# Optimization experiments

Measured on AMD Instinct MI355X. Metric: run time of the kernel, lower is better.

## Reference

```python
import jax, jax.numpy as jnp
import numpy as np

B, N, C, H = 2, 2048, 1024, 16
D = C // H  # head_dim = 64


def setup_inputs() -> dict:
    key = jax.random.key(0)
    ks = jax.random.split(key, 5)
    s = 0.02
    return {
        "x": jax.random.normal(ks[0], (B, N, C), dtype=jnp.float32),
        "w_qkv": jax.random.normal(ks[1], (3 * C, C), dtype=jnp.float32) * s,
        "b_qkv": jnp.zeros((3 * C,), dtype=jnp.float32),
        "w_proj": jax.random.normal(ks[2], (C, C), dtype=jnp.float32) * s,
        "b_proj": jnp.zeros((C,), dtype=jnp.float32),
    }


def reference(x, w_qkv, b_qkv, w_proj, b_proj):
    scale = D ** -0.5
    # QKV projection: [B,N,3C]
    qkv = jnp.einsum('bnc,oc->bno', x, w_qkv) + b_qkv
    qkv = qkv.reshape(B, N, 3, H, D).transpose(2, 0, 3, 1, 4)  # [3,B,H,N,D]
    q, k, v = qkv[0], qkv[1], qkv[2]
    attn = jnp.einsum('bhnd,bhmd->bhnm', q, k) * scale  # [B,H,N,N]
    attn = jax.nn.softmax(attn, axis=-1)
    out = jnp.einsum('bhnm,bhmd->bhnd', attn, v)  # [B,H,N,D]
    out = out.transpose(0, 2, 1, 3).reshape(B, N, C)
    return jnp.einsum('bnc,oc->bno', out, w_proj) + b_proj
```

## Files before the change

### kernel.cpp

```cpp
#include <hip/hip_runtime.h>
#include <hip/hip_bf16.h>

typedef __attribute__((ext_vector_type(4))) float f32x4;
typedef __attribute__((ext_vector_type(16))) float f32x16;
typedef __attribute__((ext_vector_type(8))) short short8;
typedef __attribute__((ext_vector_type(4))) unsigned int u32x4;
typedef __attribute__((ext_vector_type(2))) unsigned int u32x2;
typedef unsigned short u16;

__device__ __forceinline__ u16 f2bf(float x) {
  unsigned u = __float_as_uint(x);
  u += 0x7fffu + ((u >> 16) & 1u);
  return (u16)(u >> 16);
}

__device__ __forceinline__ void gload_lds16(const void* g, void* l) {
  __builtin_amdgcn_global_load_lds(
      (__attribute__((address_space(1))) void*)g,
      (__attribute__((address_space(3))) void*)l, 16, 0, 0);
}

__global__ void cvt_all(const float* __restrict__ x, const float* __restrict__ wq,
                        const float* __restrict__ wp, ushort4* __restrict__ dst) {
  const int N1 = 1048576, N2 = 786432, NT = 2097152;
  for (int i = blockIdx.x * 256 + threadIdx.x; i < NT; i += 524288) {
    float4 v;
    if (i < N1)            v = ((const float4*)x)[i];
    else if (i < N1 + N2)  v = ((const float4*)wq)[i - N1];
    else                   v = ((const float4*)wp)[i - N1 - N2];
    ushort4 o;
    o.x = f2bf(v.x); o.y = f2bf(v.y); o.z = f2bf(v.z); o.w = f2bf(v.w);
    dst[i] = o;
  }
}

__global__ __launch_bounds__(512, 2) void gemm256_bt(
    const u16* __restrict__ A, const u16* __restrict__ B,
    const float* __restrict__ bias, u16* __restrict__ Cout,
    int M, int N, int K)
{
  __shared__ u16 LA[2][2][8192];
  __shared__ u16 LB[2][12288];

  const int tid  = threadIdx.x;
  const int w    = tid >> 6;
  const int lane = tid & 63;
  const int wm   = w >> 2;
  const int wn   = w & 3;
  const int hi   = lane >> 4;
  const int lo   = lane & 15;

  const int L  = (int)(blockIdx.x & 7) * 32 + (int)(blockIdx.x >> 3);
  const int bx = L >> 4, by = L & 15;
  const long brow = (long)by * 256;
  const long bcol = (long)bx * 192;

  f32x4 acc[8][3];
#pragma unroll
  for (int m = 0; m < 8; ++m)
#pragma unroll
    for (int n = 0; n < 3; ++n)
#pragma unroll
      for (int r = 0; r < 4; ++r) acc[m][n][r] = 0.0f;

  const int srow = lane >> 3;
  const int sg   = (lane & 7) ^ srow;
  const int l7   = lo & 7;

  auto stA = [&](int kt, int bi, int i) {
    const long k0 = (long)kt * 64;
#pragma unroll
    for (int mh = 0; mh < 2; ++mh) {
      const long r = brow + mh * 128 + i * 64 + w * 8 + srow;
      gload_lds16(A + r * K + k0 + sg * 8, &LA[bi][mh][i * 4096 + w * 512]);
    }
  };
  auto stB = [&](int kt, int bi, int u) {
    const long k0 = (long)kt * 64;
    const long r = bcol + u * 64 + w * 8 + srow;
    gload_lds16(B + r * K + k0 + sg * 8, &LB[bi][u * 4096 + w * 512]);
  };

  short8 a[4][2], b[3][2];
  auto rdA = [&](int bi, int mq) {
#pragma unroll
    for (int f = 0; f < 4; ++f) {
      const int rl = mq * 64 + f * 16 + lo;
#pragma unroll
      for (int ks = 0; ks < 2; ++ks)
        a[f][ks] = *(const short8*)(&LA[bi][wm][rl * 64 + ((ks * 4 + hi) ^ l7) * 8]);
    }
  };
  auto rdB = [&](int bi) {
#pragma unroll
    for (int f = 0; f < 3; ++f) {
      const int rl = wn * 48 + f * 16 + lo;
#pragma unroll
      for (int ks = 0; ks < 2; ++ks)
        b[f][ks] = *(const short8*)(&LB[bi][rl * 64 + ((ks * 4 + hi) ^ l7) * 8]);
    }
  };

#define MFMA24(mq)                                                                  \
  __builtin_amdgcn_s_setprio(1);                                                    \
  _Pragma("unroll")                                                                 \
  for (int f = 0; f < 4; ++f)                                                       \
    _Pragma("unroll")                                                               \
    for (int n = 0; n < 3; ++n)                                                     \
      _Pragma("unroll")                                                             \
      for (int ks = 0; ks < 2; ++ks)                                                \
        acc[(mq)*4 + f][n] = __builtin_amdgcn_mfma_f32_16x16x32_bf16(               \
            a[f][ks], b[n][ks], acc[(mq)*4 + f][n], 0, 0, 0);                       \
  __builtin_amdgcn_s_setprio(0);

#define PHASE_WAIT()                                      \
  __builtin_amdgcn_s_barrier();                           \
  asm volatile("s_waitcnt lgkmcnt(0)" ::: "memory");      \
  __builtin_amdgcn_sched_barrier(0);

  const int nkt = K >> 6;
  stA(0, 0, 0); stA(0, 0, 1); stB(0, 0, 0); stB(0, 0, 1); stB(0, 0, 2);
  stA(1, 1, 0); stA(1, 1, 1); stB(1, 1, 0); stB(1, 1, 1); stB(1, 1, 2);
  asm volatile("s_waitcnt vmcnt(7)" ::: "memory");
  __builtin_amdgcn_s_barrier();

  for (int it = 0; it < (nkt >> 1); ++it) {
    const int t2 = 2 * it + 2, t3 = 2 * it + 3;
    rdA(0, 0); rdB(0);
    if (it > 0) stA(2 * it + 1, 1, 1);
    PHASE_WAIT(); MFMA24(0); __builtin_amdgcn_s_barrier();
    rdA(0, 1);
    if (t2 < nkt) { stB(t2, 0, 0); stB(t2, 0, 1); stB(t2, 0, 2); stA(t2, 0, 0); }
    PHASE_WAIT(); MFMA24(1);
    if (t2 < nkt) { asm volatile("s_waitcnt vmcnt(5)" ::: "memory"); }
    else          { asm volatile("s_waitcnt vmcnt(0)" ::: "memory"); }
    __builtin_amdgcn_sched_barrier(0);
    __builtin_amdgcn_s_barrier();
    rdA(1, 0); rdB(1);
    if (t2 < nkt) stA(t2, 0, 1);
    PHASE_WAIT(); MFMA24(0); __builtin_amdgcn_s_barrier();
    rdA(1, 1);
    if (t3 < nkt) { stB(t3, 1, 0); stB(t3, 1, 1); stB(t3, 1, 2); stA(t3, 1, 0); }
    PHASE_WAIT(); MFMA24(1);
    if (t3 < nkt) { asm volatile("s_waitcnt vmcnt(5)" ::: "memory"); }
    __builtin_amdgcn_sched_barrier(0);
    __builtin_amdgcn_s_barrier();
  }
#undef MFMA24
#undef PHASE_WAIT

  const float SCC = 0.18033688011112042f;
  float bv[3];
#pragma unroll
  for (int n = 0; n < 3; ++n) bv[n] = bias[bcol + wn * 48 + n * 16 + lo];
#pragma unroll
  for (int m = 0; m < 8; ++m)
#pragma unroll
    for (int n = 0; n < 3; ++n) {
      const long colf = bcol + wn * 48 + n * 16;
      const float qsc = (colf < 1024) ? SCC : 1.0f;
#pragma unroll
      for (int r = 0; r < 4; ++r) {
        const long row = brow + wm * 128 + m * 16 + hi * 4 + r;
        Cout[row * (long)N + colf + lo] = f2bf((acc[m][n][r] + bv[n]) * qsc);
      }
    }
}

template<int OUT_BF16>
__global__ __launch_bounds__(256) void gemm_bt(
    const u16* __restrict__ A, const u16* __restrict__ B,
    const float* __restrict__ bias, void* __restrict__ Cout,
    int M, int N, int K)
{
  __shared__ u16 As[2][128 * 64];
  __shared__ u16 Bs[2][128 * 64];
  const int tid  = threadIdx.x;
  const int lane = tid & 63;
  const int w    = tid >> 6;
  const int wm   = w >> 1, wn = w & 1;
  const int hi   = lane >> 4;
  const int lo   = lane & 15;
  const int l7   = lo & 7;
  const long brow = (long)blockIdx.y * 128;
  const long bcol = (long)blockIdx.x * 128;

  f32x4 acc[4][4];
#pragma unroll
  for (int i = 0; i < 4; i++)
#pragma unroll
    for (int j = 0; j < 4; j++)
#pragma unroll
      for (int r = 0; r < 4; r++) acc[i][j][r] = 0.0f;

  const int srow = lane >> 3;
  const int sg   = (lane & 7) ^ srow;

  float bv[4];
#pragma unroll
  for (int fn = 0; fn < 4; fn++) bv[fn] = bias[bcol + wn * 64 + fn * 16 + lo];

  auto stage = [&](int kt, int bi) {
    const int k0 = kt << 6;
#pragma unroll
    for (int c = 0; c < 4; ++c) {
      const int chunk = (c << 2) + w;
      const int ra = (chunk << 3) + srow;
      gload_lds16(A + (size_t)(brow + ra) * K + k0 + sg * 8, &As[bi][chunk * 512]);
      gload_lds16(B + (size_t)(bcol + ra) * K + k0 + sg * 8, &Bs[bi][chunk * 512]);
    }
  };

  const int nkt = K >> 6;
  stage(0, 0);
  __syncthreads();
  int cur = 0;

  for (int kt = 0; kt < nkt; ++kt) {
    if (kt + 1 < nkt) stage(kt + 1, cur ^ 1);
#pragma unroll
    for (int ks = 0; ks < 2; ++ks) {
      short8 af[4], bfr[4];
      const int g = ((ks * 4 + hi) ^ l7) * 8;
#pragma unroll
      for (int f = 0; f < 4; f++) {
        af[f]  = *(const short8*)(&As[cur][(wm * 64 + f * 16 + lo) * 64 + g]);
        bfr[f] = *(const short8*)(&Bs[cur][(wn * 64 + f * 16 + lo) * 64 + g]);
      }
#pragma unroll
      for (int fm = 0; fm < 4; fm++)
#pragma unroll
        for (int fn = 0; fn < 4; fn++)
          acc[fm][fn] = __builtin_amdgcn_mfma_f32_16x16x32_bf16(af[fm], bfr[fn], acc[fm][fn], 0, 0, 0);
    }
    __syncthreads();
    cur ^= 1;
  }

#pragma unroll
  for (int fm = 0; fm < 4; fm++)
#pragma unroll
    for (int fn = 0; fn < 4; fn++)
#pragma unroll
      for (int r = 0; r < 4; r++) {
        const long row = brow + wm * 64 + fm * 16 + hi * 4 + r;
        const long col = bcol + wn * 64 + fn * 16 + lo;
        const float v = acc[fm][fn][r] + bv[fn];
        if (OUT_BF16) ((u16*)Cout)[row * (long)N + col] = f2bf(v);
        else          ((float*)Cout)[row * (long)N + col] = v;
      }
}

__global__ __launch_bounds__(512, 4) void attn_fused(
    const u16* __restrict__ qkv, u16* __restrict__ out)
{
  __shared__ __align__(16) char smem[49152];

  const int tid  = threadIdx.x;
  const int w    = tid >> 6;
  const int lane = tid & 63;
  const int l31  = lane & 31;
  const int hc   = lane >> 5;
  const int g1   = (lane >> 4) & 1;
  const int l15  = lane & 15;
  const int half = w >> 2;
  const int qg   = w & 3;

  const int bid  = blockIdx.x;
  const int xcd  = bid & 7;
  const int slot = bid >> 3;
  const int qb   = slot & 15;
  const int bh   = ((slot >> 4) << 3) | xcd;
  const int b    = bh >> 4, h = bh & 15;

  short8 qf[4];
  {
    const u16* qp = qkv + (size_t)(b * 2048 + qb * 128 + qg * 32 + l31) * 3072 + h * 64 + hc * 8;
#pragma unroll
    for (int ds = 0; ds < 4; ++ds) qf[ds] = *(const short8*)(qp + ds * 16);
  }

  f32x16 acc0, acc1;
#pragma unroll
  for (int r = 0; r < 16; ++r) { acc0[r] = 0.f; acc1[r] = 0.f; }
  float lsum = 0.f;

  const int srow8 = lane >> 3;
  const int kgl   = (lane & 7) ^ srow8;
  const int vkey  = (lane >> 5) * 4 + ((lane >> 1) & 3);
  const int vd    = ((lane >> 3) & 3) * 16 + (lane & 1) * 8;

  auto kbuf = [&](int bi) { return (u16*)(smem + (size_t)(half * 2 + bi) * 8192); };
  u16* vb = (u16*)(smem + 32768 + (size_t)half * 8192);

  auto stK = [&](int t, int bi) {
    const size_t rbase = (size_t)(b * 2048 + half * 1024 + t * 64);
    u16* Kb = kbuf(bi);
#pragma unroll
    for (int c = 0; c < 2; ++c) {
      const int chunk = qg * 2 + c;
      gload_lds16(qkv + (rbase + chunk * 8 + srow8) * 3072 + 1024 + h * 64 + kgl * 8,
                  Kb + chunk * 512);
    }
  };
  auto stV = [&](int t) {
    const size_t rbase = (size_t)(b * 2048 + half * 1024 + t * 64);
#pragma unroll
    for (int c = 0; c < 2; ++c) {
      const int chunk = qg * 2 + c;
      gload_lds16(qkv + (rbase + chunk * 8 + vkey) * 3072 + 2048 + h * 64 + vd,
                  vb + chunk * 512);
    }
  };

  stK(0, 0); stV(0);
  asm volatile("s_waitcnt vmcnt(0)" ::: "memory");
  __builtin_amdgcn_s_barrier();
  int cur = 0;

  for (int t = 0; t < 16; ++t) {
    const bool pfK = t < 15;
    if (pfK) stK(t + 1, cur ^ 1);

    const u16* Kc = kbuf(cur);

    f32x16 s0, s1;
#pragma unroll
    for (int r = 0; r < 16; ++r) { s0[r] = 0.f; s1[r] = 0.f; }
    __builtin_amdgcn_s_setprio(1);
#pragma unroll
    for (int ds = 0; ds < 4; ++ds) {
      const int gb = (((2 * ds + hc) ^ (lane & 7)) << 4);
      const short8 k0 = *(const short8*)((const char*)Kc + l31 * 128 + gb);
      const short8 k1 = *(const short8*)((const char*)Kc + 4096 + l31 * 128 + gb);
      s0 = __builtin_amdgcn_mfma_f32_32x32x16_bf16(k0, qf[ds], s0, 0, 0, 0);
      s1 = __builtin_amdgcn_mfma_f32_32x32x16_bf16(k1, qf[ds], s1, 0, 0, 0);
    }
    __builtin_amdgcn_s_setprio(0);

    float p[32];
#pragma unroll
    for (int r = 0; r < 16; ++r) {
      p[r]      = __builtin_amdgcn_exp2f(s0[r]);
      p[16 + r] = __builtin_amdgcn_exp2f(s1[r]);
    }
    {
      float a0 = 0.f, a1 = 0.f, a2 = 0.f, a3 = 0.f;
#pragma unroll
      for (int r = 0; r < 8; ++r) {
        a0 += p[r]; a1 += p[8 + r]; a2 += p[16 + r]; a3 += p[24 + r];
      }
      lsum += (a0 + a1) + (a2 + a3);
    }

    short8 pa[4];
#pragma unroll
    for (int ks = 0; ks < 4; ++ks) {
      const int bs = ks * 8;
      unsigned X0, X1, X2, X3;
      asm("v_cvt_pk_bf16_f32 %0, %1, %2" : "=v"(X0) : "v"(p[bs + 0]), "v"(p[bs + 1]));
      asm("v_cvt_pk_bf16_f32 %0, %1, %2" : "=v"(X1) : "v"(p[bs + 2]), "v"(p[bs + 3]));
      asm("v_cvt_pk_bf16_f32 %0, %1, %2" : "=v"(X2) : "v"(p[bs + 4]), "v"(p[bs + 5]));
      asm("v_cvt_pk_bf16_f32 %0, %1, %2" : "=v"(X3) : "v"(p[bs + 6]), "v"(p[bs + 7]));
      asm("v_permlane32_swap_b32 %0, %1" : "+v"(X0), "+v"(X2));
      asm("v_permlane32_swap_b32 %0, %1" : "+v"(X1), "+v"(X3));
      u32x4 wv;
      wv[0] = X0; wv[1] = X1; wv[2] = X2; wv[3] = X3;
      pa[ks] = __builtin_bit_cast(short8, wv);
    }

    if (pfK) { asm volatile("s_waitcnt vmcnt(2)" ::: "memory"); }
    else     { asm volatile("s_waitcnt vmcnt(0)" ::: "memory"); }
    __builtin_amdgcn_sched_barrier(0);
    __builtin_amdgcn_s_barrier();

    {
      const unsigned va =
          (unsigned)(unsigned long long)(const __attribute__((address_space(3))) u16*)vb;
#pragma unroll
      for (int dt = 0; dt < 2; ++dt) {
        const unsigned vba = va + (unsigned)(hc * 1024 + dt * 256 + g1 * 128 + l15 * 8);
        u32x2 q0, q1, q2, q3, q4, q5, q6, q7;
        asm volatile("ds_read_b64_tr_b16 %0, %1"             : "=v"(q0) : "v"(vba));
        asm volatile("ds_read_b64_tr_b16 %0, %1 offset:512"  : "=v"(q1) : "v"(vba));
        asm volatile("ds_read_b64_tr_b16 %0, %1 offset:2048" : "=v"(q2) : "v"(vba));
        asm volatile("ds_read_b64_tr_b16 %0, %1 offset:2560" : "=v"(q3) : "v"(vba));
        asm volatile("ds_read_b64_tr_b16 %0, %1 offset:4096" : "=v"(q4) : "v"(vba));
        asm volatile("ds_read_b64_tr_b16 %0, %1 offset:4608" : "=v"(q5) : "v"(vba));
        asm volatile("ds_read_b64_tr_b16 %0, %1 offset:6144" : "=v"(q6) : "v"(vba));
        asm volatile("ds_read_b64_tr_b16 %0, %1 offset:6656" : "=v"(q7) : "v"(vba));
        asm volatile("s_waitcnt lgkmcnt(0)" ::: "memory");
        __builtin_amdgcn_sched_barrier(0);
        __builtin_amdgcn_s_setprio(1);
        f32x16 A = dt ? acc1 : acc0;
        {
          u32x4 bb; bb[0] = q0[0]; bb[1] = q0[1]; bb[2] = q1[0]; bb[3] = q1[1];
          A = __builtin_amdgcn_mfma_f32_32x32x16_bf16(pa[0], __builtin_bit_cast(short8, bb), A, 0, 0, 0);
        }
        {
          u32x4 bb; bb[0] = q2[0]; bb[1] = q2[1]; bb[2] = q3[0]; bb[3] = q3[1];
          A = __builtin_amdgcn_mfma_f32_32x32x16_bf16(pa[1], __builtin_bit_cast(short8, bb), A, 0, 0, 0);
        }
        {
          u32x4 bb; bb[0] = q4[0]; bb[1] = q4[1]; bb[2] = q5[0]; bb[3] = q5[1];
          A = __builtin_amdgcn_mfma_f32_32x32x16_bf16(pa[2], __builtin_bit_cast(short8, bb), A, 0, 0, 0);
        }
        {
          u32x4 bb; bb[0] = q6[0]; bb[1] = q6[1]; bb[2] = q7[0]; bb[3] = q7[1];
          A = __builtin_amdgcn_mfma_f32_32x32x16_bf16(pa[3], __builtin_bit_cast(short8, bb), A, 0, 0, 0);
        }
        __builtin_amdgcn_s_setprio(0);
        if (dt) acc1 = A; else acc0 = A;
      }
    }

    asm volatile("s_waitcnt vmcnt(0)" ::: "memory");
    __builtin_amdgcn_sched_barrier(0);
    __builtin_amdgcn_s_barrier();

    if (pfK) stV(t + 1);
    cur ^= 1;
  }

  float ltot = lsum + __shfl_xor(lsum, 32);
  float* MG = (float*)smem;
  const int midx = (qg * 64 + lane) * 33;
  if (half == 1) {
#pragma unroll
    for (int r = 0; r < 16; ++r) { MG[midx + r] = acc0[r]; MG[midx + 16 + r] = acc1[r]; }
    MG[midx + 32] = ltot;
  }
  __syncthreads();
  if (half == 0) {
#pragma unroll
    for (int r = 0; r < 16; ++r) { acc0[r] += MG[midx + r]; acc1[r] += MG[midx + 16 + r]; }
    ltot += MG[midx + 32];
    const float inv = 1.0f / ltot;
    const size_t orow0 = (size_t)(b * 2048 + qb * 128 + qg * 32);
#pragma unroll
    for (int r = 0; r < 16; ++r) {
      const int rowq = (r & 3) + 8 * (r >> 2) + 4 * hc;
      const float ir = __shfl(inv, rowq);
      out[(orow0 + rowq) * 1024 + h * 64 + l31]      = f2bf(acc0[r] * ir);
      out[(orow0 + rowq) * 1024 + h * 64 + 32 + l31] = f2bf(acc1[r] * ir);
    }
  }
}

extern "C" void kernel_launch(void* const* d_in, const int* in_sizes, int n_in,
                              void* d_out, int out_size, void* d_ws, size_t ws_size,
                              hipStream_t stream) {
  const float* x      = (const float*)d_in[0];
  const float* w_qkv  = (const float*)d_in[1];
  const float* b_qkv  = (const float*)d_in[2];
  const float* w_proj = (const float*)d_in[3];
  const float* b_proj = (const float*)d_in[4];
  float* out = (float*)d_out;

  char* ws = (char*)d_ws;
  u16* xb     = (u16*)(ws);
  u16* wqkvb  = (u16*)(ws + (8ull  << 20));
  u16* wprojb = (u16*)(ws + (14ull << 20));
  u16* qkvb   = (u16*)(ws + (16ull << 20));
  u16* aob    = (u16*)(ws + (40ull << 20));

  cvt_all<<<2048, 256, 0, stream>>>(x, w_qkv, w_proj, (ushort4*)ws);

  gemm256_bt<<<256, 512, 0, stream>>>(xb, wqkvb, b_qkv, qkvb, 4096, 3072, 1024);

  attn_fused<<<512, 512, 0, stream>>>(qkvb, aob);

  gemm_bt<0><<<dim3(8, 32), 256, 0, stream>>>(aob, wprojb, b_proj, out, 4096, 1024, 1024);
}
```

Before: 106.4 us.

## Software-pipeline attention loop: double-buffer V and overlap next QK^T with softmax/PV

Restructures the attention main loop so the V tile gets its own double buffer and the QK^T MFMAs for tile t+1 are issued before the exp/convert and PV work of tile t. K is prefetched two tiles ahead, and each iteration needs one barrier instead of two. This is meant to hide LDS and global-load latency and keep the matrix cores busy during the softmax math. In exchange, shared memory grows from 48KB to 64KB, which may lower occupancy, and the extra score accumulators raise register pressure.

```diff
diff --git a/kernel.cpp b/kernel.cpp
--- a/kernel.cpp
+++ b/kernel.cpp
@@ -254,7 +254,7 @@
 __global__ __launch_bounds__(512, 4) void attn_fused(
     const u16* __restrict__ qkv, u16* __restrict__ out)
 {
-  __shared__ __align__(16) char smem[49152];
+  __shared__ __align__(16) char smem[65536];
 
   const int tid  = threadIdx.x;
   const int w    = tid >> 6;
@@ -291,7 +291,7 @@
   const int vd    = ((lane >> 3) & 3) * 16 + (lane & 1) * 8;
 
   auto kbuf = [&](int bi) { return (u16*)(smem + (size_t)(half * 2 + bi) * 8192); };
-  u16* vb = (u16*)(smem + 32768 + (size_t)half * 8192);
+  auto vbuf = [&](int bi) { return (u16*)(smem + 32768 + (size_t)(half * 2 + bi) * 8192); };
 
   auto stK = [&](int t, int bi) {
     const size_t rbase = (size_t)(b * 2048 + half * 1024 + t * 64);
@@ -303,46 +303,55 @@
                   Kb + chunk * 512);
     }
   };
-  auto stV = [&](int t) {
+  auto stV = [&](int t, int bi) {
     const size_t rbase = (size_t)(b * 2048 + half * 1024 + t * 64);
+    u16* Vb = vbuf(bi);
 #pragma unroll
     for (int c = 0; c < 2; ++c) {
       const int chunk = qg * 2 + c;
       gload_lds16(qkv + (rbase + chunk * 8 + vkey) * 3072 + 2048 + h * 64 + vd,
-                  vb + chunk * 512);
-    }
-  };
-
-  stK(0, 0); stV(0);
-  asm volatile("s_waitcnt vmcnt(0)" ::: "memory");
-  __builtin_amdgcn_s_barrier();
-  int cur = 0;
-
-  for (int t = 0; t < 16; ++t) {
-    const bool pfK = t < 15;
-    if (pfK) stK(t + 1, cur ^ 1);
-
-    const u16* Kc = kbuf(cur);
-
-    f32x16 s0, s1;
-#pragma unroll
-    for (int r = 0; r < 16; ++r) { s0[r] = 0.f; s1[r] = 0.f; }
+                  Vb + chunk * 512);
+    }
+  };
+
+  auto qk = [&](int kr, f32x16& d0, f32x16& d1) {
+    const u16* Kc = kbuf(kr);
+#pragma unroll
+    for (int r = 0; r < 16; ++r) { d0[r] = 0.f; d1[r] = 0.f; }
     __builtin_amdgcn_s_setprio(1);
 #pragma unroll
     for (int ds = 0; ds < 4; ++ds) {
       const int gb = (((2 * ds + hc) ^ (lane & 7)) << 4);
       const short8 k0 = *(const short8*)((const char*)Kc + l31 * 128 + gb);
       const short8 k1 = *(const short8*)((const char*)Kc + 4096 + l31 * 128 + gb);
-      s0 = __builtin_amdgcn_mfma_f32_32x32x16_bf16(k0, qf[ds], s0, 0, 0, 0);
-      s1 = __builtin_amdgcn_mfma_f32_32x32x16_bf16(k1, qf[ds], s1, 0, 0, 0);
+      d0 = __builtin_amdgcn_mfma_f32_32x32x16_bf16(k0, qf[ds], d0, 0, 0, 0);
+      d1 = __builtin_amdgcn_mfma_f32_32x32x16_bf16(k1, qf[ds], d1, 0, 0, 0);
     }
     __builtin_amdgcn_s_setprio(0);
+  };
+
+  f32x16 sA0, sA1, sB0, sB1;
+
+  stK(0, 0); stV(0, 0); stK(1, 1);
+  asm volatile("s_waitcnt vmcnt(2)" ::: "memory");
+  __builtin_amdgcn_sched_barrier(0);
+  __builtin_amdgcn_s_barrier();
+  qk(0, sA0, sA1);
+
+  auto iter = [&](int T, f32x16& sC0, f32x16& sC1, f32x16& sP0, f32x16& sP1,
+                  int KD, int KR, int VR, int VD) {
+    asm volatile("s_waitcnt vmcnt(0)" ::: "memory");
+    __builtin_amdgcn_sched_barrier(0);
+    __builtin_amdgcn_s_barrier();
+    if (T + 2 <= 15) stK(T + 2, KD);
+    if (T + 1 <= 15) stV(T + 1, VD);
+    if (T + 1 <= 15) qk(KR, sP0, sP1);
 
     float p[32];
 #pragma unroll
     for (int r = 0; r < 16; ++r) {
-      p[r]      = __builtin_amdgcn_exp2f(s0[r]);
-      p[16 + r] = __builtin_amdgcn_exp2f(s1[r]);
+      p[r]      = __builtin_amdgcn_exp2f(sC0[r]);
+      p[16 + r] = __builtin_amdgcn_exp2f(sC1[r]);
     }
     {
       float a0 = 0.f, a1 = 0.f, a2 = 0.f, a3 = 0.f;
@@ -352,7 +361,6 @@
       }
       lsum += (a0 + a1) + (a2 + a3);
     }
-
     short8 pa[4];
 #pragma unroll
     for (int ks = 0; ks < 4; ++ks) {
@@ -369,14 +377,9 @@
       pa[ks] = __builtin_bit_cast(short8, wv);
     }
 
-    if (pfK) { asm volatile("s_waitcnt vmcnt(2)" ::: "memory"); }
-    else     { asm volatile("s_waitcnt vmcnt(0)" ::: "memory"); }
-    __builtin_amdgcn_sched_barrier(0);
-    __builtin_amdgcn_s_barrier();
-
     {
       const unsigned va =
-          (unsigned)(unsigned long long)(const __attribute__((address_space(3))) u16*)vb;
+          (unsigned)(unsigned long long)(const __attribute__((address_space(3))) u16*)vbuf(VR);
 #pragma unroll
       for (int dt = 0; dt < 2; ++dt) {
         const unsigned vba = va + (unsigned)(hc * 1024 + dt * 256 + g1 * 128 + l15 * 8);
@@ -413,18 +416,18 @@
         if (dt) acc1 = A; else acc0 = A;
       }
     }
-
-    asm volatile("s_waitcnt vmcnt(0)" ::: "memory");
-    __builtin_amdgcn_sched_barrier(0);
-    __builtin_amdgcn_s_barrier();
-
-    if (pfK) stV(t + 1);
-    cur ^= 1;
+  };
+
+  for (int tp = 0; tp < 8; ++tp) {
+    const int t0 = 2 * tp;
+    iter(t0,     sA0, sA1, sB0, sB1, 0, 1, 0, 1);
+    iter(t0 + 1, sB0, sB1, sA0, sA1, 1, 0, 1, 0);
   }
 
   float ltot = lsum + __shfl_xor(lsum, 32);
   float* MG = (float*)smem;
   const int midx = (qg * 64 + lane) * 33;
+  __syncthreads();
   if (half == 1) {
 #pragma unroll
     for (int r = 0; r < 16; ++r) { MG[midx + r] = acc0[r]; MG[midx + 16 + r] = acc1[r]; }
```

Result: slower. 286.9 us (+169.5%).

## Shrink QKV GEMM tile to 128x192 with simpler double-buffered pipeline

Applied to the files above, without the earlier changes.

Replaces the 256x192-tile QKV projection GEMM with a 128x192 tile, doubling the grid to 512 blocks and raising the launch-bounds occupancy hint to 4 blocks per CU. The hand-interleaved two-phase schedule is replaced by a simple per-k-tile loop that stages k-tile t+2 while computing tile t. The aim is better CU fill and latency hiding through higher occupancy. The cost is less reuse of each B tile, so more global and LDS traffic per FLOP.

```diff
diff --git a/kernel.cpp b/kernel.cpp
--- a/kernel.cpp
+++ b/kernel.cpp
@@ -34,12 +34,12 @@
   }
 }
 
-__global__ __launch_bounds__(512, 2) void gemm256_bt(
+__global__ __launch_bounds__(512, 4) void gemm128_bt(
     const u16* __restrict__ A, const u16* __restrict__ B,
     const float* __restrict__ bias, u16* __restrict__ Cout,
     int M, int N, int K)
 {
-  __shared__ u16 LA[2][2][8192];
+  __shared__ u16 LA[2][8192];
   __shared__ u16 LB[2][12288];
 
   const int tid  = threadIdx.x;
@@ -49,120 +49,93 @@
   const int wn   = w & 3;
   const int hi   = lane >> 4;
   const int lo   = lane & 15;
-
-  const int L  = (int)(blockIdx.x & 7) * 32 + (int)(blockIdx.x >> 3);
-  const int bx = L >> 4, by = L & 15;
-  const long brow = (long)by * 256;
+  const int l7   = lo & 7;
+
+  const int L  = (int)(blockIdx.x & 7) * 64 + (int)(blockIdx.x >> 3);
+  const int bx = L >> 5, by = L & 31;
+  const long brow = (long)by * 128;
   const long bcol = (long)bx * 192;
 
-  f32x4 acc[8][3];
-#pragma unroll
-  for (int m = 0; m < 8; ++m)
+  f32x4 acc[4][3];
+#pragma unroll
+  for (int f = 0; f < 4; ++f)
 #pragma unroll
     for (int n = 0; n < 3; ++n)
 #pragma unroll
-      for (int r = 0; r < 4; ++r) acc[m][n][r] = 0.0f;
+      for (int r = 0; r < 4; ++r) acc[f][n][r] = 0.0f;
 
   const int srow = lane >> 3;
   const int sg   = (lane & 7) ^ srow;
-  const int l7   = lo & 7;
-
-  auto stA = [&](int kt, int bi, int i) {
+
+  auto stage = [&](int kt, int bi) {
     const long k0 = (long)kt * 64;
 #pragma unroll
-    for (int mh = 0; mh < 2; ++mh) {
-      const long r = brow + mh * 128 + i * 64 + w * 8 + srow;
-      gload_lds16(A + r * K + k0 + sg * 8, &LA[bi][mh][i * 4096 + w * 512]);
+    for (int i = 0; i < 2; ++i) {
+      const long r = brow + i * 64 + w * 8 + srow;
+      gload_lds16(A + r * K + k0 + sg * 8, &LA[bi][i * 4096 + w * 512]);
+    }
+#pragma unroll
+    for (int u = 0; u < 3; ++u) {
+      const long r = bcol + u * 64 + w * 8 + srow;
+      gload_lds16(B + r * K + k0 + sg * 8, &LB[bi][u * 4096 + w * 512]);
     }
   };
-  auto stB = [&](int kt, int bi, int u) {
-    const long k0 = (long)kt * 64;
-    const long r = bcol + u * 64 + w * 8 + srow;
-    gload_lds16(B + r * K + k0 + sg * 8, &LB[bi][u * 4096 + w * 512]);
-  };
-
-  short8 a[4][2], b[3][2];
-  auto rdA = [&](int bi, int mq) {
+
+  const int nkt = K >> 6;
+  stage(0, 0); stage(1, 1);
+  asm volatile("s_waitcnt vmcnt(5)" ::: "memory");
+  __builtin_amdgcn_s_barrier();
+
+  for (int t = 0; t < nkt; ++t) {
+    const int bi = t & 1;
+    short8 a[4][2], b[3][2];
 #pragma unroll
     for (int f = 0; f < 4; ++f) {
-      const int rl = mq * 64 + f * 16 + lo;
+      const int rl = wm * 64 + f * 16 + lo;
 #pragma unroll
       for (int ks = 0; ks < 2; ++ks)
-        a[f][ks] = *(const short8*)(&LA[bi][wm][rl * 64 + ((ks * 4 + hi) ^ l7) * 8]);
-    }
-  };
-  auto rdB = [&](int bi) {
-#pragma unroll
-    for (int f = 0; f < 3; ++f) {
-      const int rl = wn * 48 + f * 16 + lo;
+        a[f][ks] = *(const short8*)(&LA[bi][rl * 64 + ((ks * 4 + hi) ^ l7) * 8]);
+    }
+#pragma unroll
+    for (int n = 0; n < 3; ++n) {
+      const int rl = wn * 48 + n * 16 + lo;
 #pragma unroll
       for (int ks = 0; ks < 2; ++ks)
-        b[f][ks] = *(const short8*)(&LB[bi][rl * 64 + ((ks * 4 + hi) ^ l7) * 8]);
-    }
-  };
-
-#define MFMA24(mq)                                                                  \
-  __builtin_amdgcn_s_setprio(1);                                                    \
-  _Pragma("unroll")                                                                 \
-  for (int f = 0; f < 4; ++f)                                                       \
-    _Pragma("unroll")                                                               \
-    for (int n = 0; n < 3; ++n)                                                     \
-      _Pragma("unroll")                                                             \
-      for (int ks = 0; ks < 2; ++ks)                                                \
-        acc[(mq)*4 + f][n] = __builtin_amdgcn_mfma_f32_16x16x32_bf16(               \
-            a[f][ks], b[n][ks], acc[(mq)*4 + f][n], 0, 0, 0);                       \
-  __builtin_amdgcn_s_setprio(0);
-
-#define PHASE_WAIT()                                      \
-  __builtin_amdgcn_s_barrier();                           \
-  asm volatile("s_waitcnt lgkmcnt(0)" ::: "memory");      \
-  __builtin_amdgcn_sched_barrier(0);
-
-  const int nkt = K >> 6;
-  stA(0, 0, 0); stA(0, 0, 1); stB(0, 0, 0); stB(0, 0, 1); stB(0, 0, 2);
-  stA(1, 1, 0); stA(1, 1, 1); stB(1, 1, 0); stB(1, 1, 1); stB(1, 1, 2);
-  asm volatile("s_waitcnt vmcnt(7)" ::: "memory");
-  __builtin_amdgcn_s_barrier();
-
-  for (int it = 0; it < (nkt >> 1); ++it) {
-    const int t2 = 2 * it + 2, t3 = 2 * it + 3;
-    rdA(0, 0); rdB(0);
-    if (it > 0) stA(2 * it + 1, 1, 1);
-    PHASE_WAIT(); MFMA24(0); __builtin_amdgcn_s_barrier();
-    rdA(0, 1);
-    if (t2 < nkt) { stB(t2, 0, 0); stB(t2, 0, 1); stB(t2, 0, 2); stA(t2, 0, 0); }
-    PHASE_WAIT(); MFMA24(1);
-    if (t2 < nkt) { asm volatile("s_waitcnt vmcnt(5)" ::: "memory"); }
-    else          { asm volatile("s_waitcnt vmcnt(0)" ::: "memory"); }
+        b[n][ks] = *(const short8*)(&LB[bi][rl * 64 + ((ks * 4 + hi) ^ l7) * 8]);
+    }
+    asm volatile("s_waitcnt lgkmcnt(0)" ::: "memory");
     __builtin_amdgcn_sched_barrier(0);
     __builtin_amdgcn_s_barrier();
-    rdA(1, 0); rdB(1);
-    if (t2 < nkt) stA(t2, 0, 1);
-    PHASE_WAIT(); MFMA24(0); __builtin_amdgcn_s_barrier();
-    rdA(1, 1);
-    if (t3 < nkt) { stB(t3, 1, 0); stB(t3, 1, 1); stB(t3, 1, 2); stA(t3, 1, 0); }
-    PHASE_WAIT(); MFMA24(1);
-    if (t3 < nkt) { asm volatile("s_waitcnt vmcnt(5)" ::: "memory"); }
+    if (t + 2 < nkt) stage(t + 2, bi);
+    __builtin_amdgcn_s_setprio(1);
+#pragma unroll
+    for (int f = 0; f < 4; ++f)
+#pragma unroll
+      for (int n = 0; n < 3; ++n)
+#pragma unroll
+        for (int ks = 0; ks < 2; ++ks)
+          acc[f][n] = __builtin_amdgcn_mfma_f32_16x16x32_bf16(a[f][ks], b[n][ks], acc[f][n], 0, 0, 0);
+    __builtin_amdgcn_s_setprio(0);
+    if (t + 2 < nkt)      { asm volatile("s_waitcnt vmcnt(5)" ::: "memory"); }
+    else if (t + 1 < nkt) { asm volatile("s_waitcnt vmcnt(0)" ::: "memory"); }
     __builtin_amdgcn_sched_barrier(0);
     __builtin_amdgcn_s_barrier();
   }
-#undef MFMA24
-#undef PHASE_WAIT
 
   const float SCC = 0.18033688011112042f;
   float bv[3];
 #pragma unroll
   for (int n = 0; n < 3; ++n) bv[n] = bias[bcol + wn * 48 + n * 16 + lo];
 #pragma unroll
-  for (int m = 0; m < 8; ++m)
+  for (int f = 0; f < 4; ++f)
 #pragma unroll
     for (int n = 0; n < 3; ++n) {
       const long colf = bcol + wn * 48 + n * 16;
       const float qsc = (colf < 1024) ? SCC : 1.0f;
 #pragma unroll
       for (int r = 0; r < 4; ++r) {
-        const long row = brow + wm * 128 + m * 16 + hi * 4 + r;
-        Cout[row * (long)N + colf + lo] = f2bf((acc[m][n][r] + bv[n]) * qsc);
+        const long row = brow + wm * 64 + f * 16 + hi * 4 + r;
+        Cout[row * (long)N + colf + lo] = f2bf((acc[f][n][r] + bv[n]) * qsc);
       }
     }
 }
@@ -466,7 +439,7 @@
 
   cvt_all<<<2048, 256, 0, stream>>>(x, w_qkv, w_proj, (ushort4*)ws);
 
-  gemm256_bt<<<256, 512, 0, stream>>>(xb, wqkvb, b_qkv, qkvb, 4096, 3072, 1024);
+  gemm128_bt<<<512, 512, 0, stream>>>(xb, wqkvb, b_qkv, qkvb, 4096, 3072, 1024);
 
   attn_fused<<<512, 512, 0, stream>>>(qkvb, aob);
 
```

New measurement: 105.9 us. Within noise of the previous version (-0.5%).
